# Performance work log

Hardware: AMD Instinct MI355X
Metric: run time of the kernel (lower is better)

The kernel has to match this reference:

```python
import jax, jax.numpy as jnp
import numpy as np

NEG_SLOPE = 0.2  # PyG GATConv default negative_slope


def gat_conv(x, src, dst, W, a_src, a_dst, b):
    """PyG GATConv with concat=False (mean over heads). src/dst include self-loops."""
    N = x.shape[0]
    H, C = a_src.shape
    h = (x @ W).reshape(N, H, C)                      # [N,H,C]
    alpha_src = (h * a_src).sum(-1)                   # [N,H]
    alpha_dst = (h * a_dst).sum(-1)                   # [N,H]
    e = jax.nn.leaky_relu(alpha_src[src] + alpha_dst[dst], NEG_SLOPE)  # [E,H]
    # segment softmax over incoming edges of each dst node
    emax = jax.ops.segment_max(e, dst, num_segments=N)                 # [N,H]
    ex = jnp.exp(e - emax[dst])                                        # [E,H]
    denom = jax.ops.segment_sum(ex, dst, num_segments=N)               # [N,H]
    alpha = ex / denom[dst]                                            # [E,H]
    msg = h[src] * alpha[:, :, None]                                   # [E,H,C]
    out = jax.ops.segment_sum(msg, dst, num_segments=N)                # [N,H,C]
    return out.mean(axis=1) + b                                        # concat=False -> mean heads


def setup_inputs() -> dict:
    key = jax.random.key(0)
    ks = jax.random.split(key, 16)
    N, F_IN, H, C, E = 50000, 3, 4, 64, 800000
    inp = {
        "x": jax.random.normal(ks[0], (N, F_IN), dtype=jnp.float32),
        "edge_index": jax.random.randint(ks[1], (2, E), 0, N, dtype=jnp.int32),
        "W1": jax.random.normal(ks[2], (F_IN, H * C), dtype=jnp.float32) * 0.1,
        "a1_src": jax.random.normal(ks[3], (H, C), dtype=jnp.float32) * 0.1,
        "a1_dst": jax.random.normal(ks[4], (H, C), dtype=jnp.float32) * 0.1,
        "b1": jnp.zeros((C,), dtype=jnp.float32),
        "W2": jax.random.normal(ks[5], (C, H * C), dtype=jnp.float32) * 0.1,
        "a2_src": jax.random.normal(ks[6], (H, C), dtype=jnp.float32) * 0.1,
        "a2_dst": jax.random.normal(ks[7], (H, C), dtype=jnp.float32) * 0.1,
        "b2": jnp.zeros((C,), dtype=jnp.float32),
        "W3": jax.random.normal(ks[8], (C, H * C), dtype=jnp.float32) * 0.1,
        "a3_src": jax.random.normal(ks[9], (H, C), dtype=jnp.float32) * 0.1,
        "a3_dst": jax.random.normal(ks[10], (H, C), dtype=jnp.float32) * 0.1,
        "b3": jnp.zeros((C,), dtype=jnp.float32),
        "lin_w": jax.random.normal(ks[11], (C, 1), dtype=jnp.float32) * 0.1,
        "lin_b": jnp.zeros((1,), dtype=jnp.float32),
    }
    return inp


def reference(x, edge_index, W1, a1_src, a1_dst, b1, W2, a2_src, a2_dst, b2,
              W3, a3_src, a3_dst, b3, lin_w, lin_b):
    N = x.shape[0]
    loops = jnp.arange(N, dtype=edge_index.dtype)  # PyG add_self_loops=True default
    src = jnp.concatenate([edge_index[0], loops])
    dst = jnp.concatenate([edge_index[1], loops])

    h1 = jax.nn.elu(gat_conv(x, src, dst, W1, a1_src, a1_dst, b1))
    h2 = jax.nn.elu(gat_conv(h1, src, dst, W2, a2_src, a2_dst, b2)) + h1
    h3 = jax.nn.elu(gat_conv(h2, src, dst, W3, a3_src, a3_dst, b3)) + h2
    return h3 @ lin_w + lin_b
```

## Files before the change

kernel.cpp:

```cpp
#include <hip/hip_runtime.h>
#include <math.h>

#define HEADS 4
#define CH 64
#define HC 256

typedef __attribute__((ext_vector_type(8))) short bf16x8;
typedef __attribute__((ext_vector_type(4))) float f32x4;

__device__ __forceinline__ float lrelu(float v) { return v > 0.f ? v : 0.2f * v; }

__device__ __forceinline__ unsigned int f2bf(float f) {
    unsigned int u = __float_as_uint(f);
    u += 0x7fffu + ((u >> 16) & 1u);
    return u >> 16;
}
__device__ __forceinline__ float bf2f(unsigned short u) {
    return __uint_as_float(((unsigned int)u) << 16);
}

__device__ __forceinline__ float4 wave_sum4(float4 v) {
#pragma unroll
    for (int m = 32; m; m >>= 1) {
        v.x += __shfl_xor(v.x, m);
        v.y += __shfl_xor(v.y, m);
        v.z += __shfl_xor(v.z, m);
        v.w += __shfl_xor(v.w, m);
    }
    return v;
}

__global__ void count_kernel(const int* __restrict__ dst, int E, int N,
                             float scale8, int* __restrict__ deg) {
    int r = blockIdx.x & 7;
    int e = (blockIdx.x >> 3) * blockDim.x + threadIdx.x;
    if (e >= E + N) return;
    int d = (e < E) ? dst[e] : e - E;
    int rr = min(7, (int)((float)d * scale8));
    if (rr == r) atomicAdd(&deg[d], 1);
}

__global__ void scan_blocks(const int* __restrict__ deg,
                            int* __restrict__ off,
                            int* __restrict__ bsum, int N) {
    __shared__ int sh[256];
    int t = threadIdx.x;
    int g = blockIdx.x * 256 + t;
    int v = (g < N) ? deg[g] : 0;
    sh[t] = v;
    __syncthreads();
    for (int d = 1; d < 256; d <<= 1) {
        int x = (t >= d) ? sh[t - d] : 0;
        __syncthreads();
        sh[t] += x;
        __syncthreads();
    }
    if (g < N) off[g] = sh[t] - v;
    if (t == 255) bsum[blockIdx.x] = sh[255];
}

__global__ void scan_bsums(int* __restrict__ bsum, int G,
                           int* __restrict__ total_out) {
    __shared__ int sh[256];
    int t = threadIdx.x;
    int chunk = (G + 255) / 256;
    int lo = t * chunk, hi = min(lo + chunk, G);
    int s = 0;
    for (int i = lo; i < hi; ++i) s += bsum[i];
    sh[t] = s;
    __syncthreads();
    for (int d = 1; d < 256; d <<= 1) {
        int x = (t >= d) ? sh[t - d] : 0;
        __syncthreads();
        sh[t] += x;
        __syncthreads();
    }
    int run = (t > 0) ? sh[t - 1] : 0;
    for (int i = lo; i < hi; ++i) { int v = bsum[i]; bsum[i] = run; run += v; }
    if (t == 255) *total_out = sh[255];
}

__global__ void scan_add(int* __restrict__ off, const int* __restrict__ bsum,
                         int N) {
    int g = blockIdx.x * 256 + threadIdx.x;
    if (g < N) off[g] += bsum[blockIdx.x];
}

__global__ void scatter_kernel(const int* __restrict__ src,
                               const int* __restrict__ dst, int E, int N,
                               float scale8,
                               const int* __restrict__ off,
                               int* __restrict__ cursor,
                               int* __restrict__ csr_src) {
    int r = blockIdx.x & 7;
    int e = (blockIdx.x >> 3) * blockDim.x + threadIdx.x;
    if (e >= E + N) return;
    int s, d;
    if (e < E) { s = src[e]; d = dst[e]; } else { s = d = e - E; }
    int rr = min(7, (int)((float)d * scale8));
    if (rr != r) return;
    int p = atomicAdd(&cursor[d], 1);
    csr_src[off[d] + p] = s;
}

__global__ void prep_kernel(const float* __restrict__ W,
                            const float* __restrict__ a_s,
                            const float* __restrict__ a_d,
                            unsigned short* __restrict__ Wb,
                            float* __restrict__ ws,
                            float* __restrict__ wd) {
    int b = blockIdx.x, t = threadIdx.x;
    if (b < 64) {
        Wb[b * 256 + t] = (unsigned short)f2bf(W[(t >> 2) * HC + (t & 3) * CH + b]);
    } else {
        int idx = (b - 64) * 256 + t;
        int which = idx >= 256;
        int i = which ? idx - 256 : idx;
        int k = i >> 2, h = i & 3;
        const float* av = (which ? a_d : a_s) + h * CH;
        const float* Wr = W + (size_t)k * HC + h * CH;
        float s = 0.f;
        for (int c = 0; c < CH; ++c) s += Wr[c] * av[c];
        (which ? wd : ws)[i] = s;
    }
}

__global__ void logits_kernel(const float* __restrict__ in,
                              const float* __restrict__ ws,
                              const float* __restrict__ wd,
                              float4* __restrict__ asrc4,
                              float4* __restrict__ adst4, int N) {
    int n = blockIdx.x * blockDim.x + threadIdx.x;
    if (n >= N) return;
    const float4* row = (const float4*)(in + (size_t)n * CH);
    const float4* ws4 = (const float4*)ws;
    const float4* wd4 = (const float4*)wd;
    float4 s = make_float4(0.f, 0.f, 0.f, 0.f);
    float4 d = make_float4(0.f, 0.f, 0.f, 0.f);
#pragma unroll 4
    for (int kq = 0; kq < 16; ++kq) {
        float4 x4 = row[kq];
        float xv[4] = {x4.x, x4.y, x4.z, x4.w};
#pragma unroll
        for (int dk = 0; dk < 4; ++dk) {
            float4 a = ws4[kq * 4 + dk];
            float4 c = wd4[kq * 4 + dk];
            s.x += xv[dk] * a.x; s.y += xv[dk] * a.y;
            s.z += xv[dk] * a.z; s.w += xv[dk] * a.w;
            d.x += xv[dk] * c.x; d.y += xv[dk] * c.y;
            d.z += xv[dk] * c.z; d.w += xv[dk] * c.w;
        }
    }
    asrc4[n] = s;
    adst4[n] = d;
}

__global__ void agg_kernel(const int* __restrict__ off,
                           const int* __restrict__ csr_src,
                           const unsigned short* __restrict__ xp,
                           const float4* __restrict__ asrc4,
                           const float4* __restrict__ adst4,
                           uint2* __restrict__ zb2, int N) {
    __shared__ float4 exs[4][64];
    __shared__ int    sss[4][64];
    int node = (blockIdx.x * blockDim.x + threadIdx.x) >> 6;
    int w = (threadIdx.x >> 6) & 3;
    int lane = threadIdx.x & 63;
    if (node >= N) return;
    int o0 = off[node], o1 = off[node + 1];
    int deg = o1 - o0;
    float4 ad = adst4[node];

    float l0 = 0.f, l1 = 0.f, l2 = 0.f, l3 = 0.f;
    float z0 = 0.f, z1 = 0.f, z2 = 0.f, z3 = 0.f;

    for (int base = 0; base < deg; base += 64) {
        int i = base + lane;
        int s = 0;
        float4 ev = make_float4(-INFINITY, -INFINITY, -INFINITY, -INFINITY);
        if (i < deg) {
            s = csr_src[o0 + i];
            float4 as = asrc4[s];
            ev.x = lrelu(as.x + ad.x);
            ev.y = lrelu(as.y + ad.y);
            ev.z = lrelu(as.z + ad.z);
            ev.w = lrelu(as.w + ad.w);
        }
        float4 ex;
        ex.x = __expf(ev.x);
        ex.y = __expf(ev.y);
        ex.z = __expf(ev.z);
        ex.w = __expf(ev.w);
        float4 ls = wave_sum4(ex);
        l0 += ls.x; l1 += ls.y; l2 += ls.z; l3 += ls.w;
        exs[w][lane] = ex;
        sss[w][lane] = s;

        int cnt = min(64, deg - base);
#pragma unroll 4
        for (int e = 0; e < cnt; ++e) {
            int se = sss[w][e];
            float4 exe = exs[w][e];
            float xk = bf2f(xp[(size_t)se * CH + lane]);
            z0 += exe.x * xk; z1 += exe.y * xk;
            z2 += exe.z * xk; z3 += exe.w * xk;
        }
    }
    float s0 = 0.25f / l0, s1 = 0.25f / l1, s2 = 0.25f / l2, s3 = 0.25f / l3;
    uint2 zo;
    zo.x = f2bf(z0 * s0) | (f2bf(z1 * s1) << 16);
    zo.y = f2bf(z2 * s2) | (f2bf(z3 * s3) << 16);
    zb2[(size_t)node * CH + lane] = zo;
}

__global__ void gemm_mfma(const unsigned short* __restrict__ zb,
                          const unsigned short* __restrict__ Wb,
                          const float* __restrict__ bias,
                          const float* __restrict__ residual,
                          const float* __restrict__ lin_w,
                          const float* __restrict__ lin_b,
                          float* __restrict__ out_f32,
                          unsigned short* __restrict__ out_pack,
                          float* __restrict__ out_final, int N) {
    int w = threadIdx.x >> 6;
    int lane = threadIdx.x & 63;
    int quad = lane >> 4, col = lane & 15;
    int nbase = blockIdx.x * 64 + w * 16;

    f32x4 zero4 = {0.f, 0.f, 0.f, 0.f};
    f32x4 acc[4];
#pragma unroll
    for (int t = 0; t < 4; ++t) acc[t] = zero4;

    const unsigned short* arow = zb + (size_t)(nbase + col) * HC + quad * 8;
#pragma unroll
    for (int q = 0; q < 8; ++q) {
        bf16x8 af = *(const bf16x8*)(arow + q * 32);
#pragma unroll
        for (int t = 0; t < 4; ++t) {
            const unsigned short* bp = Wb + (size_t)(t * 16 + col) * HC + q * 32 + quad * 8;
            bf16x8 bfrag = *(const bf16x8*)bp;
            acc[t] = __builtin_amdgcn_mfma_f32_16x16x32_bf16(af, bfrag, acc[t], 0, 0, 0);
        }
    }

    if (!out_final) {
#pragma unroll
        for (int t = 0; t < 4; ++t) {
            int c = t * 16 + col;
            float bc = bias[c];
#pragma unroll
            for (int r = 0; r < 4; ++r) {
                int n = nbase + quad * 4 + r;
                float v = acc[t][r] + bc;
                v = v > 0.f ? v : expm1f(v);
                v += residual[(size_t)n * CH + c];
                if (n < N) {
                    out_f32[(size_t)n * CH + c] = v;
                    out_pack[(size_t)n * CH + c] = (unsigned short)f2bf(v);
                }
            }
        }
    } else {
        float lw[4], bb[4];
#pragma unroll
        for (int t = 0; t < 4; ++t) { lw[t] = lin_w[t * 16 + col]; bb[t] = bias[t * 16 + col]; }
#pragma unroll
        for (int r = 0; r < 4; ++r) {
            int n = nbase + quad * 4 + r;
            float ts = 0.f;
#pragma unroll
            for (int t = 0; t < 4; ++t) {
                float v = acc[t][r] + bb[t];
                v = v > 0.f ? v : expm1f(v);
                v += residual[(size_t)n * CH + (t * 16 + col)];
                ts += v * lw[t];
            }
            ts += __shfl_xor(ts, 1);
            ts += __shfl_xor(ts, 2);
            ts += __shfl_xor(ts, 4);
            ts += __shfl_xor(ts, 8);
            if (col == 0 && n < N) out_final[n] = ts + lin_b[0];
        }
    }
}

__global__ void proj1_kernel(const float* __restrict__ W,
                             const float* __restrict__ a_s,
                             const float* __restrict__ a_d,
                             float* __restrict__ ws,
                             float* __restrict__ wd) {
    int t = threadIdx.x;
    for (int idx = t; idx < 24; idx += blockDim.x) {
        int which = idx >= 12;
        int i = which ? idx - 12 : idx;
        int k = i >> 2, h = i & 3;
        const float* av = (which ? a_d : a_s) + h * CH;
        const float* Wr = W + (size_t)k * HC + h * CH;
        float s = 0.f;
        for (int c = 0; c < CH; ++c) s += Wr[c] * av[c];
        (which ? wd : ws)[i] = s;
    }
}

__global__ void logits1_kernel(const float* __restrict__ x,
                               const float* __restrict__ ws,
                               const float* __restrict__ wd,
                               float4* __restrict__ asrc4,
                               float4* __restrict__ adst4, int N) {
    int n = blockIdx.x * blockDim.x + threadIdx.x;
    if (n >= N) return;
    float x0 = x[3 * n], x1 = x[3 * n + 1], x2 = x[3 * n + 2];
    float4 s4, d4;
    s4.x = x0 * ws[0] + x1 * ws[4] + x2 * ws[8];
    s4.y = x0 * ws[1] + x1 * ws[5] + x2 * ws[9];
    s4.z = x0 * ws[2] + x1 * ws[6] + x2 * ws[10];
    s4.w = x0 * ws[3] + x1 * ws[7] + x2 * ws[11];
    d4.x = x0 * wd[0] + x1 * wd[4] + x2 * wd[8];
    d4.y = x0 * wd[1] + x1 * wd[5] + x2 * wd[9];
    d4.z = x0 * wd[2] + x1 * wd[6] + x2 * wd[10];
    d4.w = x0 * wd[3] + x1 * wd[7] + x2 * wd[11];
    asrc4[n] = s4;
    adst4[n] = d4;
}

__global__ void fused1_kernel(const int* __restrict__ off,
                              const int* __restrict__ csr_src,
                              const float* __restrict__ x,
                              const float4* __restrict__ asrc4,
                              const float4* __restrict__ adst4,
                              float4* __restrict__ zl, int N) {
    int n = blockIdx.x * blockDim.x + threadIdx.x;
    if (n >= N) return;
    int o0 = off[n], o1 = off[n + 1];
    float4 ad = adst4[n];
    float z[12];
#pragma unroll
    for (int j = 0; j < 12; ++j) z[j] = 0.f;
    float l0 = 0.f, l1 = 0.f, l2 = 0.f, l3 = 0.f;

    for (int i = o0; i < o1; ++i) {
        int s = csr_src[i];
        float4 as = asrc4[s];
        float e0 = __expf(lrelu(as.x + ad.x));
        float e1 = __expf(lrelu(as.y + ad.y));
        float e2 = __expf(lrelu(as.z + ad.z));
        float e3 = __expf(lrelu(as.w + ad.w));
        l0 += e0; l1 += e1; l2 += e2; l3 += e3;
        float x0 = x[3 * s], x1 = x[3 * s + 1], x2 = x[3 * s + 2];
        z[0] += e0 * x0; z[1]  += e0 * x1; z[2]  += e0 * x2;
        z[3] += e1 * x0; z[4]  += e1 * x1; z[5]  += e1 * x2;
        z[6] += e2 * x0; z[7]  += e2 * x1; z[8]  += e2 * x2;
        z[9] += e3 * x0; z[10] += e3 * x1; z[11] += e3 * x2;
    }
    zl[(size_t)n * 4 + 0] = make_float4(z[0], z[1], z[2], z[3]);
    zl[(size_t)n * 4 + 1] = make_float4(z[4], z[5], z[6], z[7]);
    zl[(size_t)n * 4 + 2] = make_float4(z[8], z[9], z[10], z[11]);
    zl[(size_t)n * 4 + 3] = make_float4(l0, l1, l2, l3);
}

__global__ void epi1_kernel(const float4* __restrict__ zl,
                            const float* __restrict__ W1,
                            const float* __restrict__ b1,
                            const float4* __restrict__ ws2_4,
                            const float4* __restrict__ wd2_4,
                            float4* __restrict__ asrc4,
                            float4* __restrict__ adst4,
                            float* __restrict__ out,
                            unsigned short* __restrict__ out_pack, int N) {
    int node = (blockIdx.x * blockDim.x + threadIdx.x) >> 6;
    int c = threadIdx.x & 63;
    if (node >= N) return;
    float4 z0 = zl[(size_t)node * 4 + 0];
    float4 z1 = zl[(size_t)node * 4 + 1];
    float4 z2 = zl[(size_t)node * 4 + 2];
    float4 l4 = zl[(size_t)node * 4 + 3];
    float i0 = 0.25f / l4.x, i1 = 0.25f / l4.y;
    float i2 = 0.25f / l4.z, i3 = 0.25f / l4.w;
    float acc =
        (z0.x * W1[0 * HC +   0 + c] + z0.y * W1[1 * HC +   0 + c] + z0.z * W1[2 * HC +   0 + c]) * i0 +
        (z0.w * W1[0 * HC +  64 + c] + z1.x * W1[1 * HC +  64 + c] + z1.y * W1[2 * HC +  64 + c]) * i1 +
        (z1.z * W1[0 * HC + 128 + c] + z1.w * W1[1 * HC + 128 + c] + z2.x * W1[2 * HC + 128 + c]) * i2 +
        (z2.y * W1[0 * HC + 192 + c] + z2.z * W1[1 * HC + 192 + c] + z2.w * W1[2 * HC + 192 + c]) * i3;
    float v = acc + b1[c];
    v = v > 0.f ? v : expm1f(v);
    out[(size_t)node * CH + c] = v;
    out_pack[(size_t)node * CH + c] = (unsigned short)f2bf(v);
    float4 wsv = ws2_4[c], wdv = wd2_4[c];
    float4 sacc = make_float4(v * wsv.x, v * wsv.y, v * wsv.z, v * wsv.w);
    float4 dacc = make_float4(v * wdv.x, v * wdv.y, v * wdv.z, v * wdv.w);
    sacc = wave_sum4(sacc);
    dacc = wave_sum4(dacc);
    if (c == 0) { asrc4[node] = sacc; adst4[node] = dacc; }
}

extern "C" void kernel_launch(void* const* d_in, const int* in_sizes, int n_in,
                              void* d_out, int out_size, void* d_ws, size_t ws_size,
                              hipStream_t stream) {
    const float* x      = (const float*)d_in[0];
    const int*   ei     = (const int*)  d_in[1];
    const float* W1     = (const float*)d_in[2];
    const float* a1s    = (const float*)d_in[3];
    const float* a1d    = (const float*)d_in[4];
    const float* b1     = (const float*)d_in[5];
    const float* W2     = (const float*)d_in[6];
    const float* a2s    = (const float*)d_in[7];
    const float* a2d    = (const float*)d_in[8];
    const float* b2     = (const float*)d_in[9];
    const float* W3     = (const float*)d_in[10];
    const float* a3s    = (const float*)d_in[11];
    const float* a3d    = (const float*)d_in[12];
    const float* b3     = (const float*)d_in[13];
    const float* lin_w  = (const float*)d_in[14];
    const float* lin_b  = (const float*)d_in[15];

    const int N = in_sizes[0] / 3;
    const int E = in_sizes[1] / 2;
    const int Et = E + N;
    const int* src = ei;
    const int* dst = ei + E;
    const float scale8 = 8.0f / (float)N;

    unsigned short* zb  = (unsigned short*)d_ws;
    unsigned short* xpA = zb  + (size_t)N * HC;
    unsigned short* xpB = xpA + (size_t)N * CH;
    unsigned short* Wb2 = xpB + (size_t)N * CH;
    unsigned short* Wb3 = Wb2 + 16384;
    float* bufA   = (float*)(Wb3 + 16384);
    float* bufB   = bufA + (size_t)N * CH;
    float* zl     = bufB + (size_t)N * CH;
    float* asrc   = zl   + (size_t)N * 16;
    float* adst   = asrc + (size_t)N * 4;
    float* ws1    = adst + (size_t)N * 4;
    float* wd1    = ws1 + 16;
    float* ws2    = wd1 + 16;
    float* wd2    = ws2 + 256;
    float* ws3    = wd2 + 256;
    float* wd3    = ws3 + 256;
    int* deg      = (int*)(wd3 + 256);
    int* cursor   = deg + N;
    int* off      = cursor + N;
    int* bsum     = off + N + 4;
    int* csr_src  = bsum + 256;

    const int B = 256;
    const int G = (N + 255) / 256;
    const int EB = (Et + B - 1) / B;

    hipMemsetAsync(deg, 0, (size_t)2 * N * sizeof(int), stream);
    count_kernel<<<EB * 8, B, 0, stream>>>(dst, E, N, scale8, deg);
    scan_blocks<<<G, B, 0, stream>>>(deg, off, bsum, N);
    scan_bsums<<<1, B, 0, stream>>>(bsum, G, off + N);
    scan_add<<<G, B, 0, stream>>>(off, bsum, N);
    scatter_kernel<<<EB * 8, B, 0, stream>>>(src, dst, E, N, scale8,
                                             off, cursor, csr_src);

    prep_kernel<<<66, B, 0, stream>>>(W2, a2s, a2d, Wb2, ws2, wd2);
    prep_kernel<<<66, B, 0, stream>>>(W3, a3s, a3d, Wb3, ws3, wd3);

    int nwave_blocks = (N * 64 + B - 1) / B;
    int ngemm_blocks = (N + 63) / 64;

    proj1_kernel<<<1, 64, 0, stream>>>(W1, a1s, a1d, ws1, wd1);
    logits1_kernel<<<(N + B - 1) / B, B, 0, stream>>>(
        x, ws1, wd1, (float4*)asrc, (float4*)adst, N);
    fused1_kernel<<<(N + B - 1) / B, B, 0, stream>>>(
        off, csr_src, x, (const float4*)asrc, (const float4*)adst,
        (float4*)zl, N);
    epi1_kernel<<<nwave_blocks, B, 0, stream>>>(
        (const float4*)zl, W1, b1, (const float4*)ws2, (const float4*)wd2,
        (float4*)asrc, (float4*)adst, bufA, xpA, N);

    agg_kernel<<<nwave_blocks, B, 0, stream>>>(
        off, csr_src, xpA, (const float4*)asrc, (const float4*)adst,
        (uint2*)zb, N);
    gemm_mfma<<<ngemm_blocks, B, 0, stream>>>(
        zb, Wb2, b2, bufA, nullptr, nullptr, bufB, xpB, nullptr, N);

    logits_kernel<<<(N + B - 1) / B, B, 0, stream>>>(
        bufB, ws3, wd3, (float4*)asrc, (float4*)adst, N);

    agg_kernel<<<nwave_blocks, B, 0, stream>>>(
        off, csr_src, xpB, (const float4*)asrc, (const float4*)adst,
        (uint2*)zb, N);
    gemm_mfma<<<ngemm_blocks, B, 0, stream>>>(
        zb, Wb3, b3, bufB, lin_w, lin_b, nullptr, nullptr, (float*)d_out, N);
}
```

Before: 364.9 us.

## Fuse edge aggregation with MFMA projection GEMM through shared-memory tile

Merges the per-node attention aggregation kernel and the following bf16 MFMA GEMM into one 1024-thread block kernel. Each block aggregates 64 nodes into a padded LDS tile, then 16 waves each compute one 16x16 output tile from it. This removes the global write and re-read of the N x 256 bf16 intermediate and one launch per layer. In exchange it adds a block-wide barrier, so skewed degrees leave waves idle. The large block and LDS footprint may also limit occupancy.

```diff
diff --git a/kernel.cpp b/kernel.cpp
--- a/kernel.cpp
+++ b/kernel.cpp
@@ -4,6 +4,7 @@
 #define HEADS 4
 #define CH 64
 #define HC 256
+#define ZSTRIDE 264
 
 typedef __attribute__((ext_vector_type(8))) short bf16x8;
 typedef __attribute__((ext_vector_type(4))) float f32x4;
@@ -155,132 +156,127 @@
     adst4[n] = d;
 }
 
-__global__ void agg_kernel(const int* __restrict__ off,
-                           const int* __restrict__ csr_src,
-                           const unsigned short* __restrict__ xp,
-                           const float4* __restrict__ asrc4,
-                           const float4* __restrict__ adst4,
-                           uint2* __restrict__ zb2, int N) {
-    __shared__ float4 exs[4][64];
-    __shared__ int    sss[4][64];
-    int node = (blockIdx.x * blockDim.x + threadIdx.x) >> 6;
-    int w = (threadIdx.x >> 6) & 3;
+__global__ __launch_bounds__(1024) void agg_gemm(
+        const int* __restrict__ off,
+        const int* __restrict__ csr_src,
+        const unsigned short* __restrict__ xp,
+        const float4* __restrict__ asrc4,
+        const float4* __restrict__ adst4,
+        const unsigned short* __restrict__ Wb,
+        const float* __restrict__ bias,
+        const float* __restrict__ residual,
+        const float* __restrict__ lin_w,
+        const float* __restrict__ lin_b,
+        float* __restrict__ out_f32,
+        unsigned short* __restrict__ out_pack,
+        float* __restrict__ out_final, int N) {
+    __shared__ unsigned short zs[64 * ZSTRIDE];
+    __shared__ float4 exs[16][64];
+    __shared__ int    sss[16][64];
+    __shared__ float  red[64][5];
+
+    int wv = threadIdx.x >> 6;
     int lane = threadIdx.x & 63;
-    if (node >= N) return;
-    int o0 = off[node], o1 = off[node + 1];
-    int deg = o1 - o0;
-    float4 ad = adst4[node];
-
-    float l0 = 0.f, l1 = 0.f, l2 = 0.f, l3 = 0.f;
-    float z0 = 0.f, z1 = 0.f, z2 = 0.f, z3 = 0.f;
-
-    for (int base = 0; base < deg; base += 64) {
-        int i = base + lane;
-        int s = 0;
-        float4 ev = make_float4(-INFINITY, -INFINITY, -INFINITY, -INFINITY);
-        if (i < deg) {
-            s = csr_src[o0 + i];
-            float4 as = asrc4[s];
-            ev.x = lrelu(as.x + ad.x);
-            ev.y = lrelu(as.y + ad.y);
-            ev.z = lrelu(as.z + ad.z);
-            ev.w = lrelu(as.w + ad.w);
+    int nbase = blockIdx.x * 64;
+
+    for (int i = 0; i < 4; ++i) {
+        int nl = wv * 4 + i;
+        int node = nbase + nl;
+        if (node >= N) break;
+        int o0 = off[node], o1 = off[node + 1];
+        int deg = o1 - o0;
+        float4 ad = adst4[node];
+        float l0 = 0.f, l1 = 0.f, l2 = 0.f, l3 = 0.f;
+        float z0 = 0.f, z1 = 0.f, z2 = 0.f, z3 = 0.f;
+
+        for (int base = 0; base < deg; base += 64) {
+            int ii = base + lane;
+            int s = 0;
+            float4 ev = make_float4(-INFINITY, -INFINITY, -INFINITY, -INFINITY);
+            if (ii < deg) {
+                s = csr_src[o0 + ii];
+                float4 as = asrc4[s];
+                ev.x = lrelu(as.x + ad.x);
+                ev.y = lrelu(as.y + ad.y);
+                ev.z = lrelu(as.z + ad.z);
+                ev.w = lrelu(as.w + ad.w);
+            }
+            float4 ex;
+            ex.x = __expf(ev.x);
+            ex.y = __expf(ev.y);
+            ex.z = __expf(ev.z);
+            ex.w = __expf(ev.w);
+            float4 ls = wave_sum4(ex);
+            l0 += ls.x; l1 += ls.y; l2 += ls.z; l3 += ls.w;
+            exs[wv][lane] = ex;
+            sss[wv][lane] = s;
+
+            int cnt = min(64, deg - base);
+#pragma unroll 4
+            for (int e = 0; e < cnt; ++e) {
+                int se = sss[wv][e];
+                float4 exe = exs[wv][e];
+                float xk = bf2f(xp[(size_t)se * CH + lane]);
+                z0 += exe.x * xk; z1 += exe.y * xk;
+                z2 += exe.z * xk; z3 += exe.w * xk;
+            }
         }
-        float4 ex;
-        ex.x = __expf(ev.x);
-        ex.y = __expf(ev.y);
-        ex.z = __expf(ev.z);
-        ex.w = __expf(ev.w);
-        float4 ls = wave_sum4(ex);
-        l0 += ls.x; l1 += ls.y; l2 += ls.z; l3 += ls.w;
-        exs[w][lane] = ex;
-        sss[w][lane] = s;
-
-        int cnt = min(64, deg - base);
-#pragma unroll 4
-        for (int e = 0; e < cnt; ++e) {
-            int se = sss[w][e];
-            float4 exe = exs[w][e];
-            float xk = bf2f(xp[(size_t)se * CH + lane]);
-            z0 += exe.x * xk; z1 += exe.y * xk;
-            z2 += exe.z * xk; z3 += exe.w * xk;
-        }
-    }
-    float s0 = 0.25f / l0, s1 = 0.25f / l1, s2 = 0.25f / l2, s3 = 0.25f / l3;
-    uint2 zo;
-    zo.x = f2bf(z0 * s0) | (f2bf(z1 * s1) << 16);
-    zo.y = f2bf(z2 * s2) | (f2bf(z3 * s3) << 16);
-    zb2[(size_t)node * CH + lane] = zo;
-}
-
-__global__ void gemm_mfma(const unsigned short* __restrict__ zb,
-                          const unsigned short* __restrict__ Wb,
-                          const float* __restrict__ bias,
-                          const float* __restrict__ residual,
-                          const float* __restrict__ lin_w,
-                          const float* __restrict__ lin_b,
-                          float* __restrict__ out_f32,
-                          unsigned short* __restrict__ out_pack,
-                          float* __restrict__ out_final, int N) {
-    int w = threadIdx.x >> 6;
-    int lane = threadIdx.x & 63;
+        float s0 = 0.25f / l0, s1 = 0.25f / l1, s2 = 0.25f / l2, s3 = 0.25f / l3;
+        uint2 zo;
+        zo.x = f2bf(z0 * s0) | (f2bf(z1 * s1) << 16);
+        zo.y = f2bf(z2 * s2) | (f2bf(z3 * s3) << 16);
+        *(uint2*)&zs[nl * ZSTRIDE + lane * 4] = zo;
+    }
+    __syncthreads();
+
+    int rt = wv & 3, ct = wv >> 2;
     int quad = lane >> 4, col = lane & 15;
-    int nbase = blockIdx.x * 64 + w * 16;
-
-    f32x4 zero4 = {0.f, 0.f, 0.f, 0.f};
-    f32x4 acc[4];
-#pragma unroll
-    for (int t = 0; t < 4; ++t) acc[t] = zero4;
-
-    const unsigned short* arow = zb + (size_t)(nbase + col) * HC + quad * 8;
+    f32x4 acc = {0.f, 0.f, 0.f, 0.f};
+    const unsigned short* arow = zs + (rt * 16 + col) * ZSTRIDE + quad * 8;
+    const unsigned short* brow = Wb + (size_t)(ct * 16 + col) * HC + quad * 8;
 #pragma unroll
     for (int q = 0; q < 8; ++q) {
         bf16x8 af = *(const bf16x8*)(arow + q * 32);
-#pragma unroll
-        for (int t = 0; t < 4; ++t) {
-            const unsigned short* bp = Wb + (size_t)(t * 16 + col) * HC + q * 32 + quad * 8;
-            bf16x8 bfrag = *(const bf16x8*)bp;
-            acc[t] = __builtin_amdgcn_mfma_f32_16x16x32_bf16(af, bfrag, acc[t], 0, 0, 0);
-        }
-    }
-
+        bf16x8 bfrag = *(const bf16x8*)(brow + q * 32);
+        acc = __builtin_amdgcn_mfma_f32_16x16x32_bf16(af, bfrag, acc, 0, 0, 0);
+    }
+
+    int c = ct * 16 + col;
+    float bc = bias[c];
     if (!out_final) {
 #pragma unroll
-        for (int t = 0; t < 4; ++t) {
-            int c = t * 16 + col;
-            float bc = bias[c];
-#pragma unroll
-            for (int r = 0; r < 4; ++r) {
-                int n = nbase + quad * 4 + r;
-                float v = acc[t][r] + bc;
-                v = v > 0.f ? v : expm1f(v);
+        for (int r = 0; r < 4; ++r) {
+            int n = nbase + rt * 16 + quad * 4 + r;
+            float v = acc[r] + bc;
+            v = v > 0.f ? v : expm1f(v);
+            if (n < N) {
                 v += residual[(size_t)n * CH + c];
-                if (n < N) {
-                    out_f32[(size_t)n * CH + c] = v;
-                    out_pack[(size_t)n * CH + c] = (unsigned short)f2bf(v);
-                }
+                out_f32[(size_t)n * CH + c] = v;
+                out_pack[(size_t)n * CH + c] = (unsigned short)f2bf(v);
             }
         }
     } else {
-        float lw[4], bb[4];
-#pragma unroll
-        for (int t = 0; t < 4; ++t) { lw[t] = lin_w[t * 16 + col]; bb[t] = bias[t * 16 + col]; }
+        float lw = lin_w[c];
 #pragma unroll
         for (int r = 0; r < 4; ++r) {
-            int n = nbase + quad * 4 + r;
-            float ts = 0.f;
-#pragma unroll
-            for (int t = 0; t < 4; ++t) {
-                float v = acc[t][r] + bb[t];
-                v = v > 0.f ? v : expm1f(v);
-                v += residual[(size_t)n * CH + (t * 16 + col)];
-                ts += v * lw[t];
-            }
+            int n = nbase + rt * 16 + quad * 4 + r;
+            float v = acc[r] + bc;
+            v = v > 0.f ? v : expm1f(v);
+            if (n < N) v += residual[(size_t)n * CH + c];
+            float ts = v * lw;
             ts += __shfl_xor(ts, 1);
             ts += __shfl_xor(ts, 2);
             ts += __shfl_xor(ts, 4);
             ts += __shfl_xor(ts, 8);
-            if (col == 0 && n < N) out_final[n] = ts + lin_b[0];
+            if (col == 0) red[rt * 16 + quad * 4 + r][ct] = ts;
+        }
+        __syncthreads();
+        int t = threadIdx.x;
+        if (t < 64) {
+            int n = nbase + t;
+            if (n < N)
+                out_final[n] = red[t][0] + red[t][1] + red[t][2] + red[t][3]
+                               + lin_b[0];
         }
     }
 }
@@ -421,8 +417,7 @@
     const int* dst = ei + E;
     const float scale8 = 8.0f / (float)N;
 
-    unsigned short* zb  = (unsigned short*)d_ws;
-    unsigned short* xpA = zb  + (size_t)N * HC;
+    unsigned short* xpA = (unsigned short*)d_ws;
     unsigned short* xpB = xpA + (size_t)N * CH;
     unsigned short* Wb2 = xpB + (size_t)N * CH;
     unsigned short* Wb3 = Wb2 + 16384;
@@ -459,7 +454,7 @@
     prep_kernel<<<66, B, 0, stream>>>(W3, a3s, a3d, Wb3, ws3, wd3);
 
     int nwave_blocks = (N * 64 + B - 1) / B;
-    int ngemm_blocks = (N + 63) / 64;
+    int nmerge_blocks = (N + 63) / 64;
 
     proj1_kernel<<<1, 64, 0, stream>>>(W1, a1s, a1d, ws1, wd1);
     logits1_kernel<<<(N + B - 1) / B, B, 0, stream>>>(
@@ -471,18 +466,14 @@
         (const float4*)zl, W1, b1, (const float4*)ws2, (const float4*)wd2,
         (float4*)asrc, (float4*)adst, bufA, xpA, N);
 
-    agg_kernel<<<nwave_blocks, B, 0, stream>>>(
+    agg_gemm<<<nmerge_blocks, 1024, 0, stream>>>(
         off, csr_src, xpA, (const float4*)asrc, (const float4*)adst,
-        (uint2*)zb, N);
-    gemm_mfma<<<ngemm_blocks, B, 0, stream>>>(
-        zb, Wb2, b2, bufA, nullptr, nullptr, bufB, xpB, nullptr, N);
+        Wb2, b2, bufA, nullptr, nullptr, bufB, xpB, nullptr, N);
 
     logits_kernel<<<(N + B - 1) / B, B, 0, stream>>>(
         bufB, ws3, wd3, (float4*)asrc, (float4*)adst, N);
 
-    agg_kernel<<<nwave_blocks, B, 0, stream>>>(
+    agg_gemm<<<nmerge_blocks, 1024, 0, stream>>>(
         off, csr_src, xpB, (const float4*)asrc, (const float4*)adst,
-        (uint2*)zb, N);
-    gemm_mfma<<<ngemm_blocks, B, 0, stream>>>(
-        zb, Wb3, b3, bufB, lin_w, lin_b, nullptr, nullptr, (float*)d_out, N);
-}
+        Wb3, b3, bufB, lin_w, lin_b, nullptr, nullptr, (float*)d_out, N);
+}
```

After: 416.1 us. 14.0% more time.
